# Optimization experiments

Measured on AMD Instinct MI355X. Metric: run time of the kernel, lower is better.

Reference implementation:

```python
import jax, jax.numpy as jnp
import numpy as np

BATCH, SEQ, IN_DIM, OUT_DIM, N_STATE = 16, 4096, 64, 64, 512


def setup_inputs() -> dict:
    key = jax.random.key(0)
    k_x, k_a, k_b, k_c, k_d = jax.random.split(key, 5)
    x = jax.random.normal(k_x, (BATCH, SEQ, IN_DIM), dtype=jnp.float32)
    # Stable transition matrix: spectral-norm-ish scaling keeps h bounded over SEQ steps.
    A = jax.random.normal(k_a, (N_STATE, N_STATE), dtype=jnp.float32) * (0.9 / np.sqrt(N_STATE))
    B = jax.random.normal(k_b, (N_STATE, IN_DIM), dtype=jnp.float32) / np.sqrt(IN_DIM)
    C = jax.random.normal(k_c, (OUT_DIM, N_STATE), dtype=jnp.float32) / np.sqrt(N_STATE)
    D = jax.random.normal(k_d, (OUT_DIM, IN_DIM), dtype=jnp.float32) / np.sqrt(IN_DIM)
    return {"x": x, "A": A, "B": B, "C": C, "D": D}


def reference(x, A, B, C, D):
    """Linear SSM recurrence: h_t = A h_{t-1} + B x_t ; y_t = C h_t + D x_t.

    x: [batch, seq, in_dim] -> y: [batch, seq, out_dim]
    """
    batch = x.shape[0]
    n = A.shape[0]
    # Precompute input projections once (batched GEMMs outside the scan).
    bx = jnp.einsum("ni,bsi->sbn", B, x)   # [seq, batch, n_state]
    dx = jnp.einsum("oi,bsi->bso", D, x)   # [batch, seq, out_dim]

    def step(h, bx_t):
        # h: [batch, n_state]; bx_t: [batch, n_state]
        h_new = h @ A.T + bx_t
        return h_new, h_new

    h0 = jnp.zeros((batch, n), dtype=x.dtype)
    _, hs = jax.lax.scan(step, h0, bx)      # hs: [seq, batch, n_state]
    y = jnp.einsum("on,sbn->bso", C, hs) + dx
    return y
```

## Files before the change

### kernel.cpp

```cpp
#include <hip/hip_runtime.h>
#include <cstdint>
#include <cstddef>

#define BATCH 16
#define SEQ   4096
#define NS    512
#define TLAG  128
#define PADR  128
#define PS    (SEQ + PADR)
#define CTILE 128
#define XROWS (CTILE + TLAG - 1)
#define XSTR  72
#define BLK   32768

typedef unsigned short u16;
typedef unsigned int   u32;
typedef short bf16x8 __attribute__((ext_vector_type(8)));
typedef float f32x4  __attribute__((ext_vector_type(4)));

__device__ __forceinline__ u16 f2bf(float f) {
    u32 u = __builtin_bit_cast(u32, f);
    return (u16)((u + 0x7FFFu + ((u >> 16) & 1u)) >> 16);
}
__device__ __forceinline__ float bf2f(u16 h) {
    return __builtin_bit_cast(float, (u32)h << 16);
}

__global__ __launch_bounds__(256) void prep_all(const float* __restrict__ x,
                                                const float* __restrict__ A,
                                                const float* __restrict__ B,
                                                const float* __restrict__ C,
                                                u16* __restrict__ xbf,
                                                u16* __restrict__ Arm,
                                                u16* __restrict__ At,
                                                u16* __restrict__ BT,
                                                u16* __restrict__ Rt,
                                                u16* __restrict__ L)
{
    const int bid = blockIdx.x;
    if (bid < 4224) {
        const int id = bid * 256 + threadIdx.x;
        const int b   = id / (PS * 16);
        const int rem = id - b * (PS * 16);
        const int p   = rem >> 4;
        const int g   = id & 15;
        ushort4 o;
        if (p < PADR) {
            o.x = 0; o.y = 0; o.z = 0; o.w = 0;
        } else {
            const float4 v = *(const float4*)(x + ((size_t)b * SEQ + (p - PADR)) * 64 + g * 4);
            o.x = f2bf(v.x); o.y = f2bf(v.y); o.z = f2bf(v.z); o.w = f2bf(v.w);
        }
        *(ushort4*)(xbf + ((size_t)b * PS + p) * 64 + g * 4) = o;
    } else {
        const int id = (bid - 4224) * 256 + threadIdx.x;
        if (id < 262144) {
            const int r = id >> 9, c = id & 511;
            const u16 v = f2bf(A[id]);
            Arm[id] = v;
            At[(size_t)c * 512 + r] = v;
            (void)r;
        } else if (id < 262144 + 32768) {
            const int i = id - 262144;
            const int k = i >> 6, c = i & 63;
            const u16 v = f2bf(B[i]);
            BT[(size_t)c * 512 + k] = v;
            Rt[(size_t)c * 512 + k] = v;
        } else if (id < 262144 + 65536) {
            const int i = id - 262144 - 32768;
            L[i] = f2bf(C[i]);
        }
    }
}

__device__ __forceinline__ void gemm_tile(const u16* __restrict__ apM,
                                          const u16* __restrict__ bT, int n0,
                                          u16* __restrict__ oRM,
                                          u16* __restrict__ oT, int rowT,
                                          u16* __restrict__ lds)
{
    const int tid = threadIdx.x;
    const int w = tid >> 6, l = tid & 63;
    const int lr = l & 15, q8 = (l >> 4) * 8;

    const u16* ap  = apM + (size_t)(w * 16 + lr) * NS + q8;
    const u16* bp0 = bT  + (size_t)(n0 + lr) * NS + q8;

    f32x4 acc[4];
    const f32x4 zero = {0.f, 0.f, 0.f, 0.f};
    #pragma unroll
    for (int nt = 0; nt < 4; ++nt) acc[nt] = zero;

    #pragma unroll 4
    for (int ks = 0; ks < 16; ++ks) {
        const bf16x8 a = *(const bf16x8*)(ap + ks * 32);
        #pragma unroll
        for (int nt = 0; nt < 4; ++nt) {
            const bf16x8 bfr = *(const bf16x8*)(bp0 + (size_t)nt * 16 * NS + ks * 32);
            acc[nt] = __builtin_amdgcn_mfma_f32_16x16x32_bf16(a, bfr, acc[nt], 0, 0, 0);
        }
    }

    const int rr = (l >> 4) * 4;
    if (oT) {
        #pragma unroll
        for (int nt = 0; nt < 4; ++nt) {
            const int col = n0 + nt * 16 + lr;
            ushort4 pk;
            pk.x = f2bf(acc[nt][0]); pk.y = f2bf(acc[nt][1]);
            pk.z = f2bf(acc[nt][2]); pk.w = f2bf(acc[nt][3]);
            *(ushort4*)(oT + (size_t)col * NS + rowT + w * 16 + rr) = pk;
        }
    }
    if (oRM) {
        #pragma unroll
        for (int nt = 0; nt < 4; ++nt)
            #pragma unroll
            for (int r = 0; r < 4; ++r)
                lds[(w * 16 + rr + r) * 72 + nt * 16 + lr] = f2bf(acc[nt][r]);
        __syncthreads();
        const int r  = tid >> 2;
        const int c0 = (tid & 3) * 16;
        #pragma unroll
        for (int k = 0; k < 4; ++k) {
            const ushort4 q = *(const ushort4*)&lds[r * 72 + c0 + k * 4];
            *(ushort4*)(oRM + (size_t)r * NS + n0 + c0 + k * 4) = q;
        }
    }
}

__global__ __launch_bounds__(256, 1) void stage_kernel(const u16* __restrict__ expAp,
                                                       const u16* __restrict__ expBT,
                                                       u16* __restrict__ expOut,
                                                       const u16* __restrict__ sqIn,
                                                       const u16* __restrict__ sqInT,
                                                       u16* __restrict__ sqOutRM,
                                                       u16* __restrict__ sqOutT,
                                                       int E)
{
    __shared__ u16 lds[64 * 72];
    const int t = blockIdx.x;
    if (t < E) {
        const int j = t >> 3, n0 = (t & 7) * 64;
        gemm_tile(expAp + (size_t)j * BLK, expBT, n0,
                  expOut + (size_t)j * BLK, nullptr, 0, lds);
    } else {
        const int tt = t - E;
        const int mr = tt >> 3, n0 = (tt & 7) * 64;
        gemm_tile(sqIn + (size_t)mr * BLK, sqInT, n0,
                  sqOutRM + (size_t)mr * BLK, sqOutT, mr * 64, lds);
    }
}

__global__ __launch_bounds__(256, 1) void g_kernel(const u16* __restrict__ Rt,
                                                   const u16* __restrict__ L,
                                                   const float* __restrict__ D,
                                                   u16* __restrict__ Gsw)
{
    __shared__ u16 lds[64 * 72];
    const int m = blockIdx.x;
    const int q = m >> 4, r = m & 15;
    const u16* ap0 = Rt + (size_t)q * BLK;
    const u16* bT0 = L  + (size_t)r * BLK;

    const int tid = threadIdx.x;
    const int w = tid >> 6, l = tid & 63;
    const int lr = l & 15, q8 = (l >> 4) * 8;

    const u16* ap  = ap0 + (size_t)(w * 16 + lr) * NS + q8;
    const u16* bp0 = bT0 + (size_t)lr * NS + q8;

    f32x4 acc[4];
    const f32x4 zero = {0.f, 0.f, 0.f, 0.f};
    #pragma unroll
    for (int nt = 0; nt < 4; ++nt) acc[nt] = zero;

    #pragma unroll 4
    for (int ks = 0; ks < 16; ++ks) {
        const bf16x8 a = *(const bf16x8*)(ap + ks * 32);
        #pragma unroll
        for (int nt = 0; nt < 4; ++nt) {
            const bf16x8 bfr = *(const bf16x8*)(bp0 + (size_t)nt * 16 * NS + ks * 32);
            acc[nt] = __builtin_amdgcn_mfma_f32_16x16x32_bf16(a, bfr, acc[nt], 0, 0, 0);
        }
    }

    const int rr = (l >> 4) * 4;
    #pragma unroll
    for (int nt = 0; nt < 4; ++nt)
        #pragma unroll
        for (int rk = 0; rk < 4; ++rk)
            lds[(nt * 16 + lr) * 72 + (w * 16 + rr + rk)] = f2bf(acc[nt][rk]);
    __syncthreads();

    const int f = tid >> 6;
    #pragma unroll
    for (int f2 = 0; f2 < 8; f2 += 4) {
        const int fi = f2 + f;
        const int ks = fi >> 2, nt = fi & 3;
        const int o  = nt * 16 + (l & 15);
        const int i0 = ks * 32 + (l >> 4) * 8;
        u16 v[8];
        #pragma unroll
        for (int j = 0; j < 8; ++j) {
            u16 gv = lds[o * 72 + i0 + j];
            if (m == 0) gv = f2bf(bf2f(gv) + D[o * 64 + i0 + j]);
            v[j] = gv;
        }
        ushort4 p0; p0.x = v[0]; p0.y = v[1]; p0.z = v[2]; p0.w = v[3];
        ushort4 p1; p1.x = v[4]; p1.y = v[5]; p1.z = v[6]; p1.w = v[7];
        u16* dst = Gsw + ((size_t)(m * 8 + fi) * 64 + l) * 8;
        *(ushort4*)(dst + 0) = p0;
        *(ushort4*)(dst + 4) = p1;
    }
}

__global__ __launch_bounds__(256, 2) void conv_kernel(const u16* __restrict__ xbf,
                                                      const u16* __restrict__ gsw,
                                                      float* __restrict__ y)
{
    __shared__ u16 Xs[XROWS * XSTR];

    const int tid = threadIdx.x;
    const int b  = blockIdx.y;
    const int t0 = blockIdx.x * CTILE;

    {
        const int g = tid & 7;
        int r = tid >> 3;
        const u16* src = xbf + ((size_t)b * PS + t0 + 1) * 64 + g * 8;
        #pragma unroll
        for (int it = 0; it < 8; ++it, r += 32) {
            if (r < XROWS) {
                const uint4 v = *(const uint4*)(src + (size_t)r * 64);
                *(uint4*)&Xs[r * XSTR + g * 8] = v;
            }
        }
    }
    __syncthreads();

    const int w    = tid >> 6;
    const int l    = tid & 63;
    const int lr   = l & 15;
    const int q8   = (l >> 4) * 8;
    const int wrow = w * 32;

    const uint4* gp = (const uint4*)gsw + l;
    uint4 bn[8];
    #pragma unroll
    for (int f = 0; f < 8; ++f) bn[f] = gp[f * 64];

    f32x4 acc[2][4];
    const f32x4 zero = {0.f, 0.f, 0.f, 0.f};
    #pragma unroll
    for (int mt = 0; mt < 2; ++mt)
        #pragma unroll
        for (int nt = 0; nt < 4; ++nt) acc[mt][nt] = zero;

    #pragma unroll 2
    for (int m = 0; m < TLAG; ++m) {
        bf16x8 bc[8];
        #pragma unroll
        for (int f = 0; f < 8; ++f) bc[f] = __builtin_bit_cast(bf16x8, bn[f]);
        if (m < TLAG - 1) {
            const uint4* gn = gp + (size_t)(m + 1) * 512;
            #pragma unroll
            for (int f = 0; f < 8; ++f) bn[f] = gn[f * 64];
        }

        const int rbase = wrow + lr + (TLAG - 1) - m;
        bf16x8 a[2][2];
        #pragma unroll
        for (int mt = 0; mt < 2; ++mt)
            #pragma unroll
            for (int ks = 0; ks < 2; ++ks)
                a[mt][ks] = *(const bf16x8*)&Xs[(rbase + mt * 16) * XSTR + ks * 32 + q8];

        #pragma unroll
        for (int ks = 0; ks < 2; ++ks)
            #pragma unroll
            for (int mt = 0; mt < 2; ++mt)
                #pragma unroll
                for (int nt = 0; nt < 4; ++nt)
                    acc[mt][nt] = __builtin_amdgcn_mfma_f32_16x16x32_bf16(
                        a[mt][ks], bc[ks * 4 + nt], acc[mt][nt], 0, 0, 0);
    }

    const int rr = (l >> 4) * 4;
    #pragma unroll
    for (int mt = 0; mt < 2; ++mt) {
        #pragma unroll
        for (int nt = 0; nt < 4; ++nt) {
            const int t = t0 + wrow + mt * 16 + rr;
            const int o = nt * 16 + lr;
            float* yp = y + ((size_t)b * SEQ + t) * 64 + o;
            #pragma unroll
            for (int r = 0; r < 4; ++r) yp[(size_t)r * 64] = acc[mt][nt][r];
        }
    }
}

extern "C" void kernel_launch(void* const* d_in, const int* in_sizes, int n_in,
                              void* d_out, int out_size, void* d_ws, size_t ws_size,
                              hipStream_t stream)
{
    const float* x = (const float*)d_in[0];
    const float* A = (const float*)d_in[1];
    const float* B = (const float*)d_in[2];
    const float* C = (const float*)d_in[3];
    const float* D = (const float*)d_in[4];
    float* y = (float*)d_out;

    char* w = (char*)d_ws;
    u16* xbf   = (u16*)(w + 0);
    u16* Arm   = (u16*)(w + 8650752);
    u16* At    = (u16*)(w + 9175040);
    u16* A2rm  = (u16*)(w + 9699328);
    u16* A2t   = (u16*)(w + 10223616);
    u16* A4rm  = (u16*)(w + 10747904);
    u16* A4t   = (u16*)(w + 11272192);
    u16* A8rm  = (u16*)(w + 11796480);
    u16* A8t   = (u16*)(w + 12320768);
    u16* A16rm = (u16*)(w + 12845056);
    u16* A16t  = (u16*)(w + 13369344);
    u16* A32rm = (u16*)(w + 13893632);
    u16* A32t  = (u16*)(w + 14417920);
    u16* A64rm = (u16*)(w + 14942208);
    u16* BT    = (u16*)(w + 15466496);
    u16* L     = (u16*)(w + 15532032);
    u16* Rt    = (u16*)(w + 16580608);
    u16* Gsw   = (u16*)(w + 17104896);

    prep_all<<<5504, 256, 0, stream>>>(x, A, B, C, xbf, Arm, At, BT, Rt, L);

    stage_kernel<<<72, 256, 0, stream>>>(L, At, L + 1 * BLK,
                                         Arm, At, A2rm, A2t, 8);
    stage_kernel<<<80, 256, 0, stream>>>(L, A2t, L + 2 * BLK,
                                         A2rm, A2t, A4rm, A4t, 16);
    stage_kernel<<<96, 256, 0, stream>>>(L, A4t, L + 4 * BLK,
                                         A4rm, A4t, A8rm, A8t, 32);
    stage_kernel<<<128, 256, 0, stream>>>(L, A8t, L + 8 * BLK,
                                          A8rm, A8t, A16rm, A16t, 64);
    stage_kernel<<<72, 256, 0, stream>>>(Rt, A16rm, Rt + 1 * BLK,
                                         A16rm, A16t, A32rm, A32t, 8);
    stage_kernel<<<80, 256, 0, stream>>>(Rt, A32rm, Rt + 2 * BLK,
                                         A32rm, A32t, A64rm, nullptr, 16);
    stage_kernel<<<32, 256, 0, stream>>>(Rt, A64rm, Rt + 4 * BLK,
                                         nullptr, nullptr, nullptr, nullptr, 32);
    g_kernel<<<128, 256, 0, stream>>>(Rt, L, D, Gsw);

    conv_kernel<<<dim3(SEQ / CTILE, BATCH), 256, 0, stream>>>(xbf, Gsw, y);
}
```

Before: 236.8 us.

## Fuse prep and power-chain stages into one persistent kernel with per-XCD barriers

Replaces the prep kernel, the seven stage launches and the G kernel with one persistent 256-block kernel. Each XCD builds its own replicated copy of the A-power and C·A^k chain in a private arena and synchronises through atomic-counter barriers scoped to that XCD, which removes launch gaps and cross-XCD traffic. The Rt and G work is split across XCDs by ownership. The conv kernel now double-buffers the G taps in LDS instead of loading them straight from global memory each step. The cost is redundant chain compute per XCD, a large workspace requirement, and spin barriers that assume all blocks are co-resident, with the old multi-launch path kept as a fallback.

```diff
diff --git a/kernel.cpp b/kernel.cpp
--- a/kernel.cpp
+++ b/kernel.cpp
@@ -26,6 +26,442 @@
     return __builtin_bit_cast(float, (u32)h << 16);
 }
 
+__device__ __forceinline__ void gemm_tile(const u16* __restrict__ apM,
+                                          const u16* __restrict__ bT, int n0,
+                                          u16* __restrict__ oRM,
+                                          u16* __restrict__ oT, int rowT,
+                                          u16* __restrict__ lds)
+{
+    const int tid = threadIdx.x;
+    const int w = tid >> 6, l = tid & 63;
+    const int lr = l & 15, q8 = (l >> 4) * 8;
+
+    const u16* ap  = apM + (size_t)(w * 16 + lr) * NS + q8;
+    const u16* bp0 = bT  + (size_t)(n0 + lr) * NS + q8;
+
+    f32x4 acc[4];
+    const f32x4 zero = {0.f, 0.f, 0.f, 0.f};
+    #pragma unroll
+    for (int nt = 0; nt < 4; ++nt) acc[nt] = zero;
+
+    #pragma unroll 4
+    for (int ks = 0; ks < 16; ++ks) {
+        const bf16x8 a = *(const bf16x8*)(ap + ks * 32);
+        #pragma unroll
+        for (int nt = 0; nt < 4; ++nt) {
+            const bf16x8 bfr = *(const bf16x8*)(bp0 + (size_t)nt * 16 * NS + ks * 32);
+            acc[nt] = __builtin_amdgcn_mfma_f32_16x16x32_bf16(a, bfr, acc[nt], 0, 0, 0);
+        }
+    }
+
+    const int rr = (l >> 4) * 4;
+    if (oT) {
+        #pragma unroll
+        for (int nt = 0; nt < 4; ++nt) {
+            const int col = n0 + nt * 16 + lr;
+            ushort4 pk;
+            pk.x = f2bf(acc[nt][0]); pk.y = f2bf(acc[nt][1]);
+            pk.z = f2bf(acc[nt][2]); pk.w = f2bf(acc[nt][3]);
+            *(ushort4*)(oT + (size_t)col * NS + rowT + w * 16 + rr) = pk;
+        }
+    }
+    if (oRM) {
+        __syncthreads();
+        #pragma unroll
+        for (int nt = 0; nt < 4; ++nt)
+            #pragma unroll
+            for (int r = 0; r < 4; ++r)
+                lds[(w * 16 + rr + r) * 72 + nt * 16 + lr] = f2bf(acc[nt][r]);
+        __syncthreads();
+        const int r  = tid >> 2;
+        const int c0 = (tid & 3) * 16;
+        #pragma unroll
+        for (int k = 0; k < 4; ++k) {
+            const ushort4 q = *(const ushort4*)&lds[r * 72 + c0 + k * 4];
+            *(ushort4*)(oRM + (size_t)r * NS + n0 + c0 + k * 4) = q;
+        }
+    }
+}
+
+__device__ __forceinline__ void g_tile(const u16* __restrict__ ap0,
+                                       const u16* __restrict__ bT0, int m,
+                                       const float* __restrict__ D,
+                                       u16* __restrict__ Gsw,
+                                       u16* __restrict__ lds)
+{
+    const int tid = threadIdx.x;
+    const int w = tid >> 6, l = tid & 63;
+    const int lr = l & 15, q8 = (l >> 4) * 8;
+
+    const u16* ap  = ap0 + (size_t)(w * 16 + lr) * NS + q8;
+    const u16* bp0 = bT0 + (size_t)lr * NS + q8;
+
+    f32x4 acc[4];
+    const f32x4 zero = {0.f, 0.f, 0.f, 0.f};
+    #pragma unroll
+    for (int nt = 0; nt < 4; ++nt) acc[nt] = zero;
+
+    #pragma unroll 4
+    for (int ks = 0; ks < 16; ++ks) {
+        const bf16x8 a = *(const bf16x8*)(ap + ks * 32);
+        #pragma unroll
+        for (int nt = 0; nt < 4; ++nt) {
+            const bf16x8 bfr = *(const bf16x8*)(bp0 + (size_t)nt * 16 * NS + ks * 32);
+            acc[nt] = __builtin_amdgcn_mfma_f32_16x16x32_bf16(a, bfr, acc[nt], 0, 0, 0);
+        }
+    }
+
+    const int rr = (l >> 4) * 4;
+    __syncthreads();
+    #pragma unroll
+    for (int nt = 0; nt < 4; ++nt)
+        #pragma unroll
+        for (int rk = 0; rk < 4; ++rk)
+            lds[(nt * 16 + lr) * 72 + (w * 16 + rr + rk)] = f2bf(acc[nt][rk]);
+    __syncthreads();
+
+    const int f = tid >> 6;
+    #pragma unroll
+    for (int f2 = 0; f2 < 8; f2 += 4) {
+        const int fi = f2 + f;
+        const int ks = fi >> 2, nt = fi & 3;
+        const int o  = nt * 16 + (l & 15);
+        const int i0 = ks * 32 + (l >> 4) * 8;
+        u16 v[8];
+        #pragma unroll
+        for (int j = 0; j < 8; ++j) {
+            u16 gv = lds[o * 72 + i0 + j];
+            if (m == 0) gv = f2bf(bf2f(gv) + D[o * 64 + i0 + j]);
+            v[j] = gv;
+        }
+        ushort4 p0; p0.x = v[0]; p0.y = v[1]; p0.z = v[2]; p0.w = v[3];
+        ushort4 p1; p1.x = v[4]; p1.y = v[5]; p1.z = v[6]; p1.w = v[7];
+        u16* dst = Gsw + ((size_t)(m * 8 + fi) * 64 + l) * 8;
+        *(ushort4*)(dst + 0) = p0;
+        *(ushort4*)(dst + 4) = p1;
+    }
+}
+
+__device__ __forceinline__ void gbar(u32* __restrict__ f, u32 n)
+{
+    __syncthreads();
+    if (threadIdx.x == 0) {
+        __hip_atomic_fetch_add(f, 1u, __ATOMIC_RELAXED, __HIP_MEMORY_SCOPE_AGENT);
+        while (__hip_atomic_load(f, __ATOMIC_RELAXED, __HIP_MEMORY_SCOPE_AGENT) < n)
+            __builtin_amdgcn_s_sleep(2);
+    }
+    __syncthreads();
+}
+
+__device__ __forceinline__ int cnt_owned(int LG, int NG, int bit) {
+    int c = 0;
+    for (int q = LG; q < 8; q += NG) if (q & bit) ++c;
+    return c;
+}
+__device__ __forceinline__ int nth_owned(int LG, int NG, int bit, int i) {
+    int c = 0;
+    for (int q = LG; q < 8; q += NG)
+        if (q & bit) { if (c == i) return q; ++c; }
+    return 0;
+}
+
+#define AO_ARM    0
+#define AO_AT     262144
+#define AO_A2RM   524288
+#define AO_A2T    786432
+#define AO_A4RM   1048576
+#define AO_A4T    1310720
+#define AO_A8RM   1572864
+#define AO_A8T    1835008
+#define AO_A16RM  2097152
+#define AO_A16T   2359296
+#define AO_A32RM  2621440
+#define AO_A32T   2883584
+#define AO_A64RM  3145728
+#define AO_L      3407872
+#define AO_RT0    3932160
+#define AO_RTX    3964928
+#define ARENA_U16 4751360
+
+__global__ __launch_bounds__(256, 1) void chain_kernel(const float* __restrict__ x,
+                                                       const float* __restrict__ A,
+                                                       const float* __restrict__ B,
+                                                       const float* __restrict__ C,
+                                                       const float* __restrict__ D,
+                                                       u16* __restrict__ xbf,
+                                                       u16* __restrict__ arenas,
+                                                       u16* __restrict__ Gsw,
+                                                       u32* __restrict__ flg)
+{
+    __shared__ u16 lds[64 * 72];
+    __shared__ u32 sm[4];
+    const int tid = threadIdx.x;
+
+    if (tid == 0) {
+        u32 xcc;
+        asm volatile("s_getreg_b32 %0, hwreg(HW_REG_XCC_ID)" : "=s"(xcc));
+        xcc &= 7u;
+        sm[0] = xcc;
+        sm[1] = __hip_atomic_fetch_add(&flg[xcc], 1u,
+                                       __ATOMIC_RELAXED, __HIP_MEMORY_SCOPE_AGENT);
+    }
+    __syncthreads();
+    const int K = sm[0], R = sm[1];
+
+    for (int vb = blockIdx.x; vb < 4224; vb += 256) {
+        const int id = vb * 256 + tid;
+        const int b   = id / (PS * 16);
+        const int rem = id - b * (PS * 16);
+        const int p   = rem >> 4;
+        const int g   = id & 15;
+        ushort4 o;
+        if (p < PADR) {
+            o.x = 0; o.y = 0; o.z = 0; o.w = 0;
+        } else {
+            const float4 v = *(const float4*)(x + ((size_t)b * SEQ + (p - PADR)) * 64 + g * 4);
+            o.x = f2bf(v.x); o.y = f2bf(v.y); o.z = f2bf(v.z); o.w = f2bf(v.w);
+        }
+        *(ushort4*)(xbf + ((size_t)b * PS + p) * 64 + g * 4) = o;
+    }
+
+    if (tid == 0) {
+        for (;;) {
+            u32 s = 0;
+            #pragma unroll
+            for (int j = 0; j < 8; ++j)
+                s += __hip_atomic_load(&flg[j], __ATOMIC_RELAXED, __HIP_MEMORY_SCOPE_AGENT);
+            if (s == 256u) break;
+            __builtin_amdgcn_s_sleep(2);
+        }
+        u32 lg = 0, ng = 0, n = 0;
+        for (int j = 0; j < 8; ++j) {
+            const u32 cj = __hip_atomic_load(&flg[j], __ATOMIC_RELAXED, __HIP_MEMORY_SCOPE_AGENT);
+            if (cj) { if (j < K) ++lg; ++ng; }
+            if (j == K) n = cj;
+        }
+        sm[2] = n;
+        sm[3] = lg | (ng << 8);
+    }
+    __syncthreads();
+    const int N  = sm[2];
+    const int LG = sm[3] & 255;
+    const int NG = sm[3] >> 8;
+
+    u16* Gb    = arenas + (size_t)K * ARENA_U16;
+    u16* Arm   = Gb + AO_ARM;   u16* At   = Gb + AO_AT;
+    u16* A2rm  = Gb + AO_A2RM;  u16* A2t  = Gb + AO_A2T;
+    u16* A4rm  = Gb + AO_A4RM;  u16* A4t  = Gb + AO_A4T;
+    u16* A8rm  = Gb + AO_A8RM;  u16* A8t  = Gb + AO_A8T;
+    u16* A16rm = Gb + AO_A16RM; u16* A16t = Gb + AO_A16T;
+    u16* A32rm = Gb + AO_A32RM; u16* A32t = Gb + AO_A32T;
+    u16* A64rm = Gb + AO_A64RM;
+    u16* Lg    = Gb + AO_L;
+    u16* Rt0   = Gb + AO_RT0;
+    u16* RtX   = Gb + AO_RTX;
+    u32* gf    = flg + 16 + K * 8;
+
+    for (int c = R; c < 1408; c += N) {
+        const int id = c * 256 + tid;
+        if (id < 262144) {
+            const int col = id & 511;
+            const u16 v = f2bf(A[id]);
+            Arm[id] = v;
+            At[(size_t)col * 512 + (id >> 9)] = v;
+        } else if (id < 294912) {
+            const int i = id - 262144;
+            Rt0[(size_t)(i & 63) * 512 + (i >> 6)] = f2bf(B[i]);
+        } else {
+            const int i = id - 294912;
+            Lg[i] = f2bf(C[i]);
+        }
+    }
+    gbar(gf + 0, N);
+
+    {
+        const u16* sqA[4]  = {Arm, A2rm, A4rm, A8rm};
+        const u16* sqT[4]  = {At,  A2t,  A4t,  A8t};
+        u16* sqOR[4] = {A2rm, A4rm, A8rm, A16rm};
+        u16* sqOT[4] = {A2t,  A4t,  A8t,  A16t};
+        #pragma unroll 1
+        for (int lvl = 0; lvl < 4; ++lvl) {
+            const int h   = 1 << lvl;
+            const int tot = 64 + 8 * h;
+            for (int t = R; t < tot; t += N) {
+                if (t < 64) {
+                    const int mr = t >> 3, n0 = (t & 7) * 64;
+                    gemm_tile(sqA[lvl] + (size_t)mr * BLK, sqT[lvl], n0,
+                              sqOR[lvl] + (size_t)mr * BLK, sqOT[lvl], mr * 64, lds);
+                } else {
+                    const int tt = t - 64, j = tt >> 3, n0 = (tt & 7) * 64;
+                    gemm_tile(Lg + (size_t)j * BLK, sqT[lvl], n0,
+                              Lg + (size_t)(h + j) * BLK, nullptr, 0, lds);
+                }
+            }
+            gbar(gf + 1 + lvl, N);
+        }
+    }
+
+    {
+        const int c1  = cnt_owned(LG, NG, 1);
+        const int tot = 64 + 8 * c1;
+        for (int t = R; t < tot; t += N) {
+            if (t < 64) {
+                const int mr = t >> 3, n0 = (t & 7) * 64;
+                gemm_tile(A16rm + (size_t)mr * BLK, A16t, n0,
+                          A32rm + (size_t)mr * BLK, A32t, mr * 64, lds);
+            } else {
+                const int tt = t - 64, n0 = (tt & 7) * 64;
+                const int q = nth_owned(LG, NG, 1, tt >> 3);
+                gemm_tile(Rt0, A16rm, n0,
+                          RtX + ((size_t)q * 3 + 0) * BLK, nullptr, 0, lds);
+            }
+        }
+        gbar(gf + 5, N);
+    }
+
+    {
+        const int c2  = cnt_owned(LG, NG, 2);
+        const int tot = 64 + 8 * c2;
+        for (int t = R; t < tot; t += N) {
+            if (t < 64) {
+                const int mr = t >> 3, n0 = (t & 7) * 64;
+                gemm_tile(A32rm + (size_t)mr * BLK, A32t, n0,
+                          A64rm + (size_t)mr * BLK, nullptr, 0, lds);
+            } else {
+                const int tt = t - 64, n0 = (tt & 7) * 64;
+                const int q = nth_owned(LG, NG, 2, tt >> 3);
+                const u16* src = (q & 1) ? RtX + ((size_t)q * 3 + 0) * BLK : Rt0;
+                gemm_tile(src, A32rm, n0,
+                          RtX + ((size_t)q * 3 + 1) * BLK, nullptr, 0, lds);
+            }
+        }
+        gbar(gf + 6, N);
+    }
+
+    {
+        const int c4  = cnt_owned(LG, NG, 4);
+        for (int t = R; t < 8 * c4; t += N) {
+            const int n0 = (t & 7) * 64;
+            const int q = nth_owned(LG, NG, 4, t >> 3);
+            const u16* src = (q & 2) ? RtX + ((size_t)q * 3 + 1) * BLK
+                           : (q & 1) ? RtX + ((size_t)q * 3 + 0) * BLK : Rt0;
+            gemm_tile(src, A64rm, n0,
+                      RtX + ((size_t)q * 3 + 2) * BLK, nullptr, 0, lds);
+        }
+        gbar(gf + 7, N);
+    }
+
+    {
+        const int nq = (8 - LG + NG - 1) / NG;
+        for (int t = R; t < 16 * nq; t += N) {
+            const int q = LG + (t >> 4) * NG;
+            const int r = t & 15;
+            const u16* rf = (q & 4) ? RtX + ((size_t)q * 3 + 2) * BLK
+                          : (q & 2) ? RtX + ((size_t)q * 3 + 1) * BLK
+                          : (q & 1) ? RtX + ((size_t)q * 3 + 0) * BLK : Rt0;
+            g_tile(rf, Lg + (size_t)r * BLK, 16 * q + r, D, Gsw, lds);
+        }
+    }
+}
+
+__global__ __launch_bounds__(256, 2) void conv_kernel(const u16* __restrict__ xbf,
+                                                      const u16* __restrict__ gsw,
+                                                      float* __restrict__ y)
+{
+    __shared__ u16 Xs[XROWS * XSTR];
+    __shared__ uint4 Gs[2][1024];
+
+    const int tid = threadIdx.x;
+    const int b  = blockIdx.y;
+    const int t0 = blockIdx.x * CTILE;
+
+    {
+        const int g = tid & 7;
+        int r = tid >> 3;
+        const u16* src = xbf + ((size_t)b * PS + t0 + 1) * 64 + g * 8;
+        #pragma unroll
+        for (int it = 0; it < 8; ++it, r += 32) {
+            if (r < XROWS) {
+                const uint4 v = *(const uint4*)(src + (size_t)r * 64);
+                *(uint4*)&Xs[r * XSTR + g * 8] = v;
+            }
+        }
+    }
+
+    const uint4* gp4 = (const uint4*)gsw;
+    uint4 st[4];
+    #pragma unroll
+    for (int j = 0; j < 4; ++j) st[j] = gp4[tid + j * 256];
+
+    const int w    = tid >> 6;
+    const int l    = tid & 63;
+    const int lr   = l & 15;
+    const int q8   = (l >> 4) * 8;
+    const int wrow = w * 32;
+
+    f32x4 acc[2][4];
+    const f32x4 zero = {0.f, 0.f, 0.f, 0.f};
+    #pragma unroll
+    for (int mt = 0; mt < 2; ++mt)
+        #pragma unroll
+        for (int nt = 0; nt < 4; ++nt) acc[mt][nt] = zero;
+
+    #pragma unroll
+    for (int j = 0; j < 4; ++j) Gs[0][tid + j * 256] = st[j];
+    __syncthreads();
+
+    for (int p = 0; p < 64; ++p) {
+        const int cur = p & 1;
+        if (p < 63) {
+            #pragma unroll
+            for (int j = 0; j < 4; ++j) st[j] = gp4[(p + 1) * 1024 + tid + j * 256];
+        }
+        #pragma unroll
+        for (int sub = 0; sub < 2; ++sub) {
+            const int m = 2 * p + sub;
+            bf16x8 bc[8];
+            #pragma unroll
+            for (int f = 0; f < 8; ++f)
+                bc[f] = __builtin_bit_cast(bf16x8, Gs[cur][sub * 512 + f * 64 + l]);
+
+            const int rbase = wrow + lr + (TLAG - 1) - m;
+            bf16x8 a[2][2];
+            #pragma unroll
+            for (int mt = 0; mt < 2; ++mt)
+                #pragma unroll
+                for (int ks = 0; ks < 2; ++ks)
+                    a[mt][ks] = *(const bf16x8*)&Xs[(rbase + mt * 16) * XSTR + ks * 32 + q8];
+
+            #pragma unroll
+            for (int ks = 0; ks < 2; ++ks)
+                #pragma unroll
+                for (int mt = 0; mt < 2; ++mt)
+                    #pragma unroll
+                    for (int nt = 0; nt < 4; ++nt)
+                        acc[mt][nt] = __builtin_amdgcn_mfma_f32_16x16x32_bf16(
+                            a[mt][ks], bc[ks * 4 + nt], acc[mt][nt], 0, 0, 0);
+        }
+        if (p < 63) {
+            #pragma unroll
+            for (int j = 0; j < 4; ++j) Gs[cur ^ 1][tid + j * 256] = st[j];
+        }
+        __syncthreads();
+    }
+
+    const int rr = (l >> 4) * 4;
+    #pragma unroll
+    for (int mt = 0; mt < 2; ++mt) {
+        #pragma unroll
+        for (int nt = 0; nt < 4; ++nt) {
+            const int t = t0 + wrow + mt * 16 + rr;
+            const int o = nt * 16 + lr;
+            float* yp = y + ((size_t)b * SEQ + t) * 64 + o;
+            #pragma unroll
+            for (int r = 0; r < 4; ++r) yp[(size_t)r * 64] = acc[mt][nt][r];
+        }
+    }
+}
+
 __global__ __launch_bounds__(256) void prep_all(const float* __restrict__ x,
                                                 const float* __restrict__ A,
                                                 const float* __restrict__ B,
@@ -33,7 +469,6 @@
                                                 u16* __restrict__ xbf,
                                                 u16* __restrict__ Arm,
                                                 u16* __restrict__ At,
-                                                u16* __restrict__ BT,
                                                 u16* __restrict__ Rt,
                                                 u16* __restrict__ L)
 {
@@ -55,76 +490,16 @@
     } else {
         const int id = (bid - 4224) * 256 + threadIdx.x;
         if (id < 262144) {
-            const int r = id >> 9, c = id & 511;
+            const int c = id & 511;
             const u16 v = f2bf(A[id]);
             Arm[id] = v;
-            At[(size_t)c * 512 + r] = v;
-            (void)r;
+            At[(size_t)c * 512 + (id >> 9)] = v;
         } else if (id < 262144 + 32768) {
             const int i = id - 262144;
-            const int k = i >> 6, c = i & 63;
-            const u16 v = f2bf(B[i]);
-            BT[(size_t)c * 512 + k] = v;
-            Rt[(size_t)c * 512 + k] = v;
+            Rt[(size_t)(i & 63) * 512 + (i >> 6)] = f2bf(B[i]);
         } else if (id < 262144 + 65536) {
             const int i = id - 262144 - 32768;
             L[i] = f2bf(C[i]);
-        }
-    }
-}
-
-__device__ __forceinline__ void gemm_tile(const u16* __restrict__ apM,
-                                          const u16* __restrict__ bT, int n0,
-                                          u16* __restrict__ oRM,
-                                          u16* __restrict__ oT, int rowT,
-                                          u16* __restrict__ lds)
-{
-    const int tid = threadIdx.x;
-    const int w = tid >> 6, l = tid & 63;
-    const int lr = l & 15, q8 = (l >> 4) * 8;
-
-    const u16* ap  = apM + (size_t)(w * 16 + lr) * NS + q8;
-    const u16* bp0 = bT  + (size_t)(n0 + lr) * NS + q8;
-
-    f32x4 acc[4];
-    const f32x4 zero = {0.f, 0.f, 0.f, 0.f};
-    #pragma unroll
-    for (int nt = 0; nt < 4; ++nt) acc[nt] = zero;
-
-    #pragma unroll 4
-    for (int ks = 0; ks < 16; ++ks) {
-        const bf16x8 a = *(const bf16x8*)(ap + ks * 32);
-        #pragma unroll
-        for (int nt = 0; nt < 4; ++nt) {
-            const bf16x8 bfr = *(const bf16x8*)(bp0 + (size_t)nt * 16 * NS + ks * 32);
-            acc[nt] = __builtin_amdgcn_mfma_f32_16x16x32_bf16(a, bfr, acc[nt], 0, 0, 0);
-        }
-    }
-
-    const int rr = (l >> 4) * 4;
-    if (oT) {
-        #pragma unroll
-        for (int nt = 0; nt < 4; ++nt) {
-            const int col = n0 + nt * 16 + lr;
-            ushort4 pk;
-            pk.x = f2bf(acc[nt][0]); pk.y = f2bf(acc[nt][1]);
-            pk.z = f2bf(acc[nt][2]); pk.w = f2bf(acc[nt][3]);
-            *(ushort4*)(oT + (size_t)col * NS + rowT + w * 16 + rr) = pk;
-        }
-    }
-    if (oRM) {
-        #pragma unroll
-        for (int nt = 0; nt < 4; ++nt)
-            #pragma unroll
-            for (int r = 0; r < 4; ++r)
-                lds[(w * 16 + rr + r) * 72 + nt * 16 + lr] = f2bf(acc[nt][r]);
-        __syncthreads();
-        const int r  = tid >> 2;
-        const int c0 = (tid & 3) * 16;
-        #pragma unroll
-        for (int k = 0; k < 4; ++k) {
-            const ushort4 q = *(const ushort4*)&lds[r * 72 + c0 + k * 4];
-            *(ushort4*)(oRM + (size_t)r * NS + n0 + c0 + k * 4) = q;
         }
     }
 }
@@ -159,145 +534,7 @@
 {
     __shared__ u16 lds[64 * 72];
     const int m = blockIdx.x;
-    const int q = m >> 4, r = m & 15;
-    const u16* ap0 = Rt + (size_t)q * BLK;
-    const u16* bT0 = L  + (size_t)r * BLK;
-
-    const int tid = threadIdx.x;
-    const int w = tid >> 6, l = tid & 63;
-    const int lr = l & 15, q8 = (l >> 4) * 8;
-
-    const u16* ap  = ap0 + (size_t)(w * 16 + lr) * NS + q8;
-    const u16* bp0 = bT0 + (size_t)lr * NS + q8;
-
-    f32x4 acc[4];
-    const f32x4 zero = {0.f, 0.f, 0.f, 0.f};
-    #pragma unroll
-    for (int nt = 0; nt < 4; ++nt) acc[nt] = zero;
-
-    #pragma unroll 4
-    for (int ks = 0; ks < 16; ++ks) {
-        const bf16x8 a = *(const bf16x8*)(ap + ks * 32);
-        #pragma unroll
-        for (int nt = 0; nt < 4; ++nt) {
-            const bf16x8 bfr = *(const bf16x8*)(bp0 + (size_t)nt * 16 * NS + ks * 32);
-            acc[nt] = __builtin_amdgcn_mfma_f32_16x16x32_bf16(a, bfr, acc[nt], 0, 0, 0);
-        }
-    }
-
-    const int rr = (l >> 4) * 4;
-    #pragma unroll
-    for (int nt = 0; nt < 4; ++nt)
-        #pragma unroll
-        for (int rk = 0; rk < 4; ++rk)
-            lds[(nt * 16 + lr) * 72 + (w * 16 + rr + rk)] = f2bf(acc[nt][rk]);
-    __syncthreads();
-
-    const int f = tid >> 6;
-    #pragma unroll
-    for (int f2 = 0; f2 < 8; f2 += 4) {
-        const int fi = f2 + f;
-        const int ks = fi >> 2, nt = fi & 3;
-        const int o  = nt * 16 + (l & 15);
-        const int i0 = ks * 32 + (l >> 4) * 8;
-        u16 v[8];
-        #pragma unroll
-        for (int j = 0; j < 8; ++j) {
-            u16 gv = lds[o * 72 + i0 + j];
-            if (m == 0) gv = f2bf(bf2f(gv) + D[o * 64 + i0 + j]);
-            v[j] = gv;
-        }
-        ushort4 p0; p0.x = v[0]; p0.y = v[1]; p0.z = v[2]; p0.w = v[3];
-        ushort4 p1; p1.x = v[4]; p1.y = v[5]; p1.z = v[6]; p1.w = v[7];
-        u16* dst = Gsw + ((size_t)(m * 8 + fi) * 64 + l) * 8;
-        *(ushort4*)(dst + 0) = p0;
-        *(ushort4*)(dst + 4) = p1;
-    }
-}
-
-__global__ __launch_bounds__(256, 2) void conv_kernel(const u16* __restrict__ xbf,
-                                                      const u16* __restrict__ gsw,
-                                                      float* __restrict__ y)
-{
-    __shared__ u16 Xs[XROWS * XSTR];
-
-    const int tid = threadIdx.x;
-    const int b  = blockIdx.y;
-    const int t0 = blockIdx.x * CTILE;
-
-    {
-        const int g = tid & 7;
-        int r = tid >> 3;
-        const u16* src = xbf + ((size_t)b * PS + t0 + 1) * 64 + g * 8;
-        #pragma unroll
-        for (int it = 0; it < 8; ++it, r += 32) {
-            if (r < XROWS) {
-                const uint4 v = *(const uint4*)(src + (size_t)r * 64);
-                *(uint4*)&Xs[r * XSTR + g * 8] = v;
-            }
-        }
-    }
-    __syncthreads();
-
-    const int w    = tid >> 6;
-    const int l    = tid & 63;
-    const int lr   = l & 15;
-    const int q8   = (l >> 4) * 8;
-    const int wrow = w * 32;
-
-    const uint4* gp = (const uint4*)gsw + l;
-    uint4 bn[8];
-    #pragma unroll
-    for (int f = 0; f < 8; ++f) bn[f] = gp[f * 64];
-
-    f32x4 acc[2][4];
-    const f32x4 zero = {0.f, 0.f, 0.f, 0.f};
-    #pragma unroll
-    for (int mt = 0; mt < 2; ++mt)
-        #pragma unroll
-        for (int nt = 0; nt < 4; ++nt) acc[mt][nt] = zero;
-
-    #pragma unroll 2
-    for (int m = 0; m < TLAG; ++m) {
-        bf16x8 bc[8];
-        #pragma unroll
-        for (int f = 0; f < 8; ++f) bc[f] = __builtin_bit_cast(bf16x8, bn[f]);
-        if (m < TLAG - 1) {
-            const uint4* gn = gp + (size_t)(m + 1) * 512;
-            #pragma unroll
-            for (int f = 0; f < 8; ++f) bn[f] = gn[f * 64];
-        }
-
-        const int rbase = wrow + lr + (TLAG - 1) - m;
-        bf16x8 a[2][2];
-        #pragma unroll
-        for (int mt = 0; mt < 2; ++mt)
-            #pragma unroll
-            for (int ks = 0; ks < 2; ++ks)
-                a[mt][ks] = *(const bf16x8*)&Xs[(rbase + mt * 16) * XSTR + ks * 32 + q8];
-
-        #pragma unroll
-        for (int ks = 0; ks < 2; ++ks)
-            #pragma unroll
-            for (int mt = 0; mt < 2; ++mt)
-                #pragma unroll
-                for (int nt = 0; nt < 4; ++nt)
-                    acc[mt][nt] = __builtin_amdgcn_mfma_f32_16x16x32_bf16(
-                        a[mt][ks], bc[ks * 4 + nt], acc[mt][nt], 0, 0, 0);
-    }
-
-    const int rr = (l >> 4) * 4;
-    #pragma unroll
-    for (int mt = 0; mt < 2; ++mt) {
-        #pragma unroll
-        for (int nt = 0; nt < 4; ++nt) {
-            const int t = t0 + wrow + mt * 16 + rr;
-            const int o = nt * 16 + lr;
-            float* yp = y + ((size_t)b * SEQ + t) * 64 + o;
-            #pragma unroll
-            for (int r = 0; r < 4; ++r) yp[(size_t)r * 64] = acc[mt][nt][r];
-        }
-    }
+    g_tile(Rt + (size_t)(m >> 4) * BLK, L + (size_t)(m & 15) * BLK, m, D, Gsw, lds);
 }
 
 extern "C" void kernel_launch(void* const* d_in, const int* in_sizes, int n_in,
@@ -310,44 +547,47 @@
     const float* C = (const float*)d_in[3];
     const float* D = (const float*)d_in[4];
     float* y = (float*)d_out;
-
     char* w = (char*)d_ws;
-    u16* xbf   = (u16*)(w + 0);
-    u16* Arm   = (u16*)(w + 8650752);
-    u16* At    = (u16*)(w + 9175040);
-    u16* A2rm  = (u16*)(w + 9699328);
-    u16* A2t   = (u16*)(w + 10223616);
-    u16* A4rm  = (u16*)(w + 10747904);
-    u16* A4t   = (u16*)(w + 11272192);
-    u16* A8rm  = (u16*)(w + 11796480);
-    u16* A8t   = (u16*)(w + 12320768);
-    u16* A16rm = (u16*)(w + 12845056);
-    u16* A16t  = (u16*)(w + 13369344);
-    u16* A32rm = (u16*)(w + 13893632);
-    u16* A32t  = (u16*)(w + 14417920);
-    u16* A64rm = (u16*)(w + 14942208);
-    u16* BT    = (u16*)(w + 15466496);
-    u16* L     = (u16*)(w + 15532032);
-    u16* Rt    = (u16*)(w + 16580608);
-    u16* Gsw   = (u16*)(w + 17104896);
-
-    prep_all<<<5504, 256, 0, stream>>>(x, A, B, C, xbf, Arm, At, BT, Rt, L);
-
-    stage_kernel<<<72, 256, 0, stream>>>(L, At, L + 1 * BLK,
-                                         Arm, At, A2rm, A2t, 8);
-    stage_kernel<<<80, 256, 0, stream>>>(L, A2t, L + 2 * BLK,
-                                         A2rm, A2t, A4rm, A4t, 16);
-    stage_kernel<<<96, 256, 0, stream>>>(L, A4t, L + 4 * BLK,
-                                         A4rm, A4t, A8rm, A8t, 32);
-    stage_kernel<<<128, 256, 0, stream>>>(L, A8t, L + 8 * BLK,
-                                          A8rm, A8t, A16rm, A16t, 64);
-    stage_kernel<<<72, 256, 0, stream>>>(Rt, A16rm, Rt + 1 * BLK,
-                                         A16rm, A16t, A32rm, A32t, 8);
-    stage_kernel<<<80, 256, 0, stream>>>(Rt, A32rm, Rt + 2 * BLK,
-                                         A32rm, A32t, A64rm, nullptr, 16);
-    stage_kernel<<<32, 256, 0, stream>>>(Rt, A64rm, Rt + 4 * BLK,
-                                         nullptr, nullptr, nullptr, nullptr, 32);
-    g_kernel<<<128, 256, 0, stream>>>(Rt, L, D, Gsw);
-
-    conv_kernel<<<dim3(SEQ / CTILE, BATCH), 256, 0, stream>>>(xbf, Gsw, y);
-}
+
+    const size_t WS_NEED_FUSED = 9699840ull + 8ull * 9502720ull;
+
+    if (ws_size >= WS_NEED_FUSED) {
+        u16* xbf    = (u16*)(w + 0);
+        u16* Gsw    = (u16*)(w + 8650752);
+        u32* flg    = (u32*)(w + 9699328);
+        u16* arenas = (u16*)(w + 9699840);
+
+        hipMemsetAsync(flg, 0, 512, stream);
+        chain_kernel<<<256, 256, 0, stream>>>(x, A, B, C, D, xbf, arenas, Gsw, flg);
+        conv_kernel<<<dim3(SEQ / CTILE, BATCH), 256, 0, stream>>>(xbf, Gsw, y);
+    } else {
+        u16* xbf   = (u16*)(w + 0);
+        u16* Arm   = (u16*)(w + 8650752);
+        u16* At    = (u16*)(w + 9175040);
+        u16* A2rm  = (u16*)(w + 9699328);
+        u16* A2t   = (u16*)(w + 10223616);
+        u16* A4rm  = (u16*)(w + 10747904);
+        u16* A4t   = (u16*)(w + 11272192);
+        u16* A8rm  = (u16*)(w + 11796480);
+        u16* A8t   = (u16*)(w + 12320768);
+        u16* A16rm = (u16*)(w + 12845056);
+        u16* A16t  = (u16*)(w + 13369344);
+        u16* A32rm = (u16*)(w + 13893632);
+        u16* A32t  = (u16*)(w + 14417920);
+        u16* A64rm = (u16*)(w + 14942208);
+        u16* L     = (u16*)(w + 15532032);
+        u16* Rt    = (u16*)(w + 16580608);
+        u16* Gsw   = (u16*)(w + 17104896);
+
+        prep_all<<<5504, 256, 0, stream>>>(x, A, B, C, xbf, Arm, At, Rt, L);
+        stage_kernel<<<72, 256, 0, stream>>>(L, At, L + 1 * BLK, Arm, At, A2rm, A2t, 8);
+        stage_kernel<<<80, 256, 0, stream>>>(L, A2t, L + 2 * BLK, A2rm, A2t, A4rm, A4t, 16);
+        stage_kernel<<<96, 256, 0, stream>>>(L, A4t, L + 4 * BLK, A4rm, A4t, A8rm, A8t, 32);
+        stage_kernel<<<128, 256, 0, stream>>>(L, A8t, L + 8 * BLK, A8rm, A8t, A16rm, A16t, 64);
+        stage_kernel<<<72, 256, 0, stream>>>(Rt, A16rm, Rt + 1 * BLK, A16rm, A16t, A32rm, A32t, 8);
+        stage_kernel<<<80, 256, 0, stream>>>(Rt, A32rm, Rt + 2 * BLK, A32rm, A32t, A64rm, nullptr, 16);
+        stage_kernel<<<32, 256, 0, stream>>>(Rt, A64rm, Rt + 4 * BLK, nullptr, nullptr, nullptr, nullptr, 32);
+        g_kernel<<<128, 256, 0, stream>>>(Rt, L, D, Gsw);
+        conv_kernel<<<dim3(SEQ / CTILE, BATCH), 256, 0, stream>>>(xbf, Gsw, y);
+    }
+}
```

Measured after the change: 385.0 us. 1.63x slower.

## Stage convolution filter taps through double-buffered LDS shared across waves

Applied to the files above, without the earlier changes.

The conv kernel used to have every wave load all filter-tap fragments straight from global memory, one tap per iteration, so the same data was read redundantly by each of the four waves. It now loads two taps per step cooperatively into a double-buffered LDS array, prefetching the next pair into registers while the current pair feeds the MFMAs. This cuts global/L2 traffic fourfold, but adds a block-wide barrier every two taps and 32 KB more LDS per block, which may limit occupancy. Separately, the unused BT transpose write is dropped from the prep kernel.

```diff
diff --git a/kernel.cpp b/kernel.cpp
--- a/kernel.cpp
+++ b/kernel.cpp
@@ -33,7 +33,6 @@
                                                 u16* __restrict__ xbf,
                                                 u16* __restrict__ Arm,
                                                 u16* __restrict__ At,
-                                                u16* __restrict__ BT,
                                                 u16* __restrict__ Rt,
                                                 u16* __restrict__ L)
 {
@@ -55,17 +54,13 @@
     } else {
         const int id = (bid - 4224) * 256 + threadIdx.x;
         if (id < 262144) {
-            const int r = id >> 9, c = id & 511;
+            const int c = id & 511;
             const u16 v = f2bf(A[id]);
             Arm[id] = v;
-            At[(size_t)c * 512 + r] = v;
-            (void)r;
+            At[(size_t)c * 512 + (id >> 9)] = v;
         } else if (id < 262144 + 32768) {
             const int i = id - 262144;
-            const int k = i >> 6, c = i & 63;
-            const u16 v = f2bf(B[i]);
-            BT[(size_t)c * 512 + k] = v;
-            Rt[(size_t)c * 512 + k] = v;
+            Rt[(size_t)(i & 63) * 512 + (i >> 6)] = f2bf(B[i]);
         } else if (id < 262144 + 65536) {
             const int i = id - 262144 - 32768;
             L[i] = f2bf(C[i]);
@@ -220,6 +215,7 @@
                                                       float* __restrict__ y)
 {
     __shared__ u16 Xs[XROWS * XSTR];
+    __shared__ uint4 Gs[2][1024];
 
     const int tid = threadIdx.x;
     const int b  = blockIdx.y;
@@ -237,7 +233,11 @@
             }
         }
     }
-    __syncthreads();
+
+    const uint4* gp4 = (const uint4*)gsw;
+    uint4 st[4];
+    #pragma unroll
+    for (int j = 0; j < 4; ++j) st[j] = gp4[tid + j * 256];
 
     const int w    = tid >> 6;
     const int l    = tid & 63;
@@ -245,11 +245,6 @@
     const int q8   = (l >> 4) * 8;
     const int wrow = w * 32;
 
-    const uint4* gp = (const uint4*)gsw + l;
-    uint4 bn[8];
-    #pragma unroll
-    for (int f = 0; f < 8; ++f) bn[f] = gp[f * 64];
-
     f32x4 acc[2][4];
     const f32x4 zero = {0.f, 0.f, 0.f, 0.f};
     #pragma unroll
@@ -257,33 +252,46 @@
         #pragma unroll
         for (int nt = 0; nt < 4; ++nt) acc[mt][nt] = zero;
 
-    #pragma unroll 2
-    for (int m = 0; m < TLAG; ++m) {
-        bf16x8 bc[8];
-        #pragma unroll
-        for (int f = 0; f < 8; ++f) bc[f] = __builtin_bit_cast(bf16x8, bn[f]);
-        if (m < TLAG - 1) {
-            const uint4* gn = gp + (size_t)(m + 1) * 512;
-            #pragma unroll
-            for (int f = 0; f < 8; ++f) bn[f] = gn[f * 64];
-        }
-
-        const int rbase = wrow + lr + (TLAG - 1) - m;
-        bf16x8 a[2][2];
-        #pragma unroll
-        for (int mt = 0; mt < 2; ++mt)
-            #pragma unroll
-            for (int ks = 0; ks < 2; ++ks)
-                a[mt][ks] = *(const bf16x8*)&Xs[(rbase + mt * 16) * XSTR + ks * 32 + q8];
-
-        #pragma unroll
-        for (int ks = 0; ks < 2; ++ks)
+    #pragma unroll
+    for (int j = 0; j < 4; ++j) Gs[0][tid + j * 256] = st[j];
+    __syncthreads();
+
+    for (int p = 0; p < 64; ++p) {
+        const int cur = p & 1;
+        if (p < 63) {
+            #pragma unroll
+            for (int j = 0; j < 4; ++j) st[j] = gp4[(p + 1) * 1024 + tid + j * 256];
+        }
+        #pragma unroll
+        for (int sub = 0; sub < 2; ++sub) {
+            const int m = 2 * p + sub;
+            bf16x8 bc[8];
+            #pragma unroll
+            for (int f = 0; f < 8; ++f)
+                bc[f] = __builtin_bit_cast(bf16x8, Gs[cur][sub * 512 + f * 64 + l]);
+
+            const int rbase = wrow + lr + (TLAG - 1) - m;
+            bf16x8 a[2][2];
             #pragma unroll
             for (int mt = 0; mt < 2; ++mt)
                 #pragma unroll
-                for (int nt = 0; nt < 4; ++nt)
-                    acc[mt][nt] = __builtin_amdgcn_mfma_f32_16x16x32_bf16(
-                        a[mt][ks], bc[ks * 4 + nt], acc[mt][nt], 0, 0, 0);
+                for (int ks = 0; ks < 2; ++ks)
+                    a[mt][ks] = *(const bf16x8*)&Xs[(rbase + mt * 16) * XSTR + ks * 32 + q8];
+
+            #pragma unroll
+            for (int ks = 0; ks < 2; ++ks)
+                #pragma unroll
+                for (int mt = 0; mt < 2; ++mt)
+                    #pragma unroll
+                    for (int nt = 0; nt < 4; ++nt)
+                        acc[mt][nt] = __builtin_amdgcn_mfma_f32_16x16x32_bf16(
+                            a[mt][ks], bc[ks * 4 + nt], acc[mt][nt], 0, 0, 0);
+        }
+        if (p < 63) {
+            #pragma unroll
+            for (int j = 0; j < 4; ++j) Gs[cur ^ 1][tid + j * 256] = st[j];
+        }
+        __syncthreads();
     }
 
     const int rr = (l >> 4) * 4;
@@ -326,12 +334,11 @@
     u16* A32rm = (u16*)(w + 13893632);
     u16* A32t  = (u16*)(w + 14417920);
     u16* A64rm = (u16*)(w + 14942208);
-    u16* BT    = (u16*)(w + 15466496);
     u16* L     = (u16*)(w + 15532032);
     u16* Rt    = (u16*)(w + 16580608);
     u16* Gsw   = (u16*)(w + 17104896);
 
-    prep_all<<<5504, 256, 0, stream>>>(x, A, B, C, xbf, Arm, At, BT, Rt, L);
+    prep_all<<<5504, 256, 0, stream>>>(x, A, B, C, xbf, Arm, At, Rt, L);
 
     stage_kernel<<<72, 256, 0, stream>>>(L, At, L + 1 * BLK,
                                          Arm, At, A2rm, A2t, 8);
```

New measurement: 235.3 us. Within noise of the previous version (-0.7%).
